# Kernel tuning notes

Hardware: AMD Instinct MI355X
Metric: run time of the kernel (lower is better)

The kernel has to match this reference:

```python
import jax, jax.numpy as jnp
import numpy as np
from jax.ops import segment_max, segment_sum

N_NODES = 50000
N_EDGES = 800000
IN_CH = 256
HEADS = 8
OUT_CH = 32
NEG_SLOPE = 0.2
EPS = 1e-16


def setup_inputs() -> dict:
    key = jax.random.key(0)
    k1, k2, k3, k4, k5 = jax.random.split(key, 5)
    x = jax.random.normal(k1, (N_NODES, IN_CH), dtype=jnp.float32)
    edge_index = jax.random.randint(k2, (2, N_EDGES), 0, N_NODES, dtype=jnp.int64)
    # params (xavier-ish scale)
    W = jax.random.normal(k3, (HEADS * OUT_CH, IN_CH), dtype=jnp.float32) * (1.0 / np.sqrt(IN_CH))
    a_left = jax.random.normal(k4, (HEADS, OUT_CH), dtype=jnp.float32) * (1.0 / np.sqrt(OUT_CH))
    a_right = jax.random.normal(k5, (HEADS, OUT_CH), dtype=jnp.float32) * (1.0 / np.sqrt(OUT_CH))
    return {"x": x, "edge_index": edge_index, "W": W, "a_left": a_left, "a_right": a_right}


def reference(x, edge_index, W, a_left, a_right):
    N = x.shape[0]
    H, C = HEADS, OUT_CH
    # add self loops
    loops = jnp.arange(N, dtype=edge_index.dtype)
    src = jnp.concatenate([edge_index[0], loops])
    dst = jnp.concatenate([edge_index[1], loops])
    # Wh: [N, H, C]
    Wh = (x @ W.T).reshape(N, H, C)
    # per-node attention halves: [N, H]
    e_left = jnp.einsum('nhc,hc->nh', Wh, a_left)
    e_right = jnp.einsum('nhc,hc->nh', Wh, a_right)
    # per-edge score: [E, H]
    e = e_left[src] + e_right[dst]
    e = jnp.where(e >= 0, e, NEG_SLOPE * e)
    # segment softmax over edges grouped by dst
    e_max = segment_max(e, dst, num_segments=N)
    e_max = jnp.where(jnp.isfinite(e_max), e_max, 0.0)
    e_exp = jnp.exp(e - e_max[dst])
    denom = segment_sum(e_exp, dst, num_segments=N)
    alpha = e_exp / (denom[dst] + EPS)
    # scatter-add aggregation: [N, H, C]
    out = segment_sum(Wh[src] * alpha[:, :, None], dst, num_segments=N)
    return out.reshape(N, H * C)
```

## Files before the change

kernel.cpp:

```cpp
#include <hip/hip_runtime.h>
#include <hip/hip_bf16.h>

#define N_NODES 50000
#define N_EDGES 800000
#define IN_CH 256
#define HEADS 8
#define OUT_CH 32
#define HC 256
#define E_TOT (N_EDGES + N_NODES)
#define NEG_SLOPE 0.2f

typedef short s16x8 __attribute__((ext_vector_type(8)));
typedef float f32x4 __attribute__((ext_vector_type(4)));

__device__ __forceinline__ unsigned short f2bf(float f) {
    unsigned int u = __float_as_uint(f);
    unsigned int r = (u + 0x7FFFu + ((u >> 16) & 1u)) >> 16;
    return (unsigned short)r;
}
__device__ __forceinline__ float bf2f(unsigned short b) {
    return __uint_as_float(((unsigned int)b) << 16);
}

__device__ __forceinline__ int tbyte(int r, int k2) { return (r * 64 + k2) ^ ((r & 7) << 4); }

__global__ __launch_bounds__(512) void gemm_kernel(const float* __restrict__ x,
                                                   const float* __restrict__ W,
                                                   const float* __restrict__ a_left,
                                                   const float* __restrict__ a_right,
                                                   unsigned short* __restrict__ Wh,
                                                   float* __restrict__ el,
                                                   float* __restrict__ er) {
    __shared__ unsigned short As[64 * 32];
    __shared__ unsigned short Bs[256 * 32];
    char* Asb = (char*)As;
    char* Bsb = (char*)Bs;
    const int m0 = blockIdx.x * 64;
    const int t  = threadIdx.x;
    const int l  = t & 63;
    const int wv = t >> 6;
    const int wr = wv & 3;
    const int wc = wv >> 1 >> 1;
    const int c16  = l & 15;
    const int rgrp = l >> 4;

    f32x4 acc[8];
#pragma unroll
    for (int i = 0; i < 8; ++i) acc[i] = (f32x4){0.f, 0.f, 0.f, 0.f};

    for (int k0 = 0; k0 < IN_CH; k0 += 32) {
        {
            int r = t >> 3, kq = (t & 7) << 2;
            float4 v = make_float4(0.f, 0.f, 0.f, 0.f);
            if (m0 + r < N_NODES) v = *(const float4*)&x[(size_t)(m0 + r) * IN_CH + k0 + kq];
            ushort4 o; o.x = f2bf(v.x); o.y = f2bf(v.y); o.z = f2bf(v.z); o.w = f2bf(v.w);
            *(ushort4*)(Asb + tbyte(r, kq * 2)) = o;
        }
        {
            int r = t >> 1, kq = (t & 1) << 4;
            const float* wp = &W[(size_t)r * IN_CH + k0 + kq];
            float4 v0 = *(const float4*)(wp + 0);
            float4 v1 = *(const float4*)(wp + 4);
            float4 v2 = *(const float4*)(wp + 8);
            float4 v3 = *(const float4*)(wp + 12);
            ushort4 o0, o1, o2, o3;
            o0.x = f2bf(v0.x); o0.y = f2bf(v0.y); o0.z = f2bf(v0.z); o0.w = f2bf(v0.w);
            o1.x = f2bf(v1.x); o1.y = f2bf(v1.y); o1.z = f2bf(v1.z); o1.w = f2bf(v1.w);
            o2.x = f2bf(v2.x); o2.y = f2bf(v2.y); o2.z = f2bf(v2.z); o2.w = f2bf(v2.w);
            o3.x = f2bf(v3.x); o3.y = f2bf(v3.y); o3.z = f2bf(v3.z); o3.w = f2bf(v3.w);
            int b0 = kq * 2;
            *(ushort4*)(Bsb + tbyte(r, b0 + 0))  = o0;
            *(ushort4*)(Bsb + tbyte(r, b0 + 8))  = o1;
            *(ushort4*)(Bsb + tbyte(r, b0 + 16)) = o2;
            *(ushort4*)(Bsb + tbyte(r, b0 + 24)) = o3;
        }
        __syncthreads();
        s16x8 af = *(const s16x8*)(Asb + tbyte(wr * 16 + c16, rgrp * 16));
#pragma unroll
        for (int nt = 0; nt < 8; ++nt) {
            s16x8 bf = *(const s16x8*)(Bsb + tbyte(wc * 128 + nt * 16 + c16, rgrp * 16));
            acc[nt] = __builtin_amdgcn_mfma_f32_16x16x32_bf16(af, bf, acc[nt], 0, 0, 0);
        }
        __syncthreads();
    }

#pragma unroll
    for (int hp = 0; hp < 4; ++hp) {
        int hg  = wc * 4 + hp;
        int nt0 = hp * 2;
        float al0 = a_left [hg * OUT_CH + c16];
        float al1 = a_left [hg * OUT_CH + 16 + c16];
        float ar0 = a_right[hg * OUT_CH + c16];
        float ar1 = a_right[hg * OUT_CH + 16 + c16];
#pragma unroll
        for (int rg = 0; rg < 4; ++rg) {
            float pl = acc[nt0][rg] * al0 + acc[nt0 + 1][rg] * al1;
            float pr = acc[nt0][rg] * ar0 + acc[nt0 + 1][rg] * ar1;
#pragma unroll
            for (int m = 1; m < 16; m <<= 1) {
                pl += __shfl_xor(pl, m, 16);
                pr += __shfl_xor(pr, m, 16);
            }
            int row = m0 + wr * 16 + rgrp * 4 + rg;
            if (c16 == 0 && row < N_NODES) {
                el[row * HEADS + hg] = pl;
                er[row * HEADS + hg] = pr;
            }
        }
    }
#pragma unroll
    for (int nt = 0; nt < 8; ++nt) {
#pragma unroll
        for (int rg = 0; rg < 4; ++rg) {
            int row = m0 + wr * 16 + rgrp * 4 + rg;
            if (row < N_NODES)
                Wh[(size_t)row * HC + wc * 128 + nt * 16 + c16] = f2bf(acc[nt][rg]);
        }
    }
}

__global__ void zero_kernel(int* __restrict__ p, int n) {
    int i = blockIdx.x * blockDim.x + threadIdx.x;
    if (i < n) p[i] = 0;
}

__global__ void hist_kernel(const int* __restrict__ src, const int* __restrict__ dst,
                            int* __restrict__ count) {
    int e = blockIdx.x * blockDim.x + threadIdx.x;
    if (e >= E_TOT) return;
    int s, d;
    if (e < N_EDGES) { s = src[e]; d = dst[e]; } else { s = d = e - N_EDGES; }
    if ((unsigned)s >= N_NODES || (unsigned)d >= N_NODES) return;
    atomicAdd(&count[d], 1);
}

__global__ __launch_bounds__(1024) void scan_kernel(const int* __restrict__ count,
                                                    int* __restrict__ offset,
                                                    int* __restrict__ cursor) {
    __shared__ int wtot[16];
    __shared__ int wbase[16];
    __shared__ int running_s;
    int t = threadIdx.x, lane = t & 63, wid = t >> 6;
    if (t == 0) running_s = 0;
    __syncthreads();
    for (int base = 0; base < N_NODES; base += 1024) {
        int idx = base + t;
        int v = (idx < N_NODES) ? count[idx] : 0;
        int s = v;
#pragma unroll
        for (int off = 1; off < 64; off <<= 1) {
            int u = __shfl_up(s, off, 64);
            if (lane >= off) s += u;
        }
        if (lane == 63) wtot[wid] = s;
        __syncthreads();
        if (t == 0) {
            int b = running_s;
            for (int w = 0; w < 16; ++w) { wbase[w] = b; b += wtot[w]; }
            running_s = b;
        }
        __syncthreads();
        int excl = s - v + wbase[wid];
        if (idx < N_NODES) { offset[idx] = excl; cursor[idx] = excl; }
        __syncthreads();
    }
    if (t == 0) offset[N_NODES] = running_s;
}

__global__ void scatter_kernel(const int* __restrict__ src, const int* __restrict__ dst,
                               int* __restrict__ cursor, int* __restrict__ srcs) {
    int e = blockIdx.x * blockDim.x + threadIdx.x;
    if (e >= E_TOT) return;
    int s, d;
    if (e < N_EDGES) { s = src[e]; d = dst[e]; } else { s = d = e - N_EDGES; }
    if ((unsigned)s >= N_NODES || (unsigned)d >= N_NODES) return;
    int pos = atomicAdd(&cursor[d], 1);
    srcs[pos] = s;
}

__global__ __launch_bounds__(256) void agg_kernel(const unsigned short* __restrict__ Wh,
                                                  const float* __restrict__ el,
                                                  const float* __restrict__ er,
                                                  const int* __restrict__ offset,
                                                  const int* __restrict__ srcs,
                                                  float* __restrict__ out) {
    int n = blockIdx.x;
    int t = threadIdx.x;
    int h = t >> 5;
    float ern = er[n * HEADS + h];
    int start = offset[n], end = offset[n + 1];
    float acc = 0.f, den = 0.f;
    int j = start;
    for (; j + 4 <= end; j += 4) {
        int s0 = srcs[j + 0], s1 = srcs[j + 1], s2 = srcs[j + 2], s3 = srcs[j + 3];
        float w0 = bf2f(Wh[(size_t)s0 * HC + t]);
        float w1 = bf2f(Wh[(size_t)s1 * HC + t]);
        float w2 = bf2f(Wh[(size_t)s2 * HC + t]);
        float w3 = bf2f(Wh[(size_t)s3 * HC + t]);
        float sc0 = el[s0 * HEADS + h] + ern;
        float sc1 = el[s1 * HEADS + h] + ern;
        float sc2 = el[s2 * HEADS + h] + ern;
        float sc3 = el[s3 * HEADS + h] + ern;
        sc0 = fmaxf(sc0, NEG_SLOPE * sc0);
        sc1 = fmaxf(sc1, NEG_SLOPE * sc1);
        sc2 = fmaxf(sc2, NEG_SLOPE * sc2);
        sc3 = fmaxf(sc3, NEG_SLOPE * sc3);
        float e0 = __expf(sc0), e1 = __expf(sc1), e2 = __expf(sc2), e3 = __expf(sc3);
        acc = fmaf(e0, w0, acc);
        acc = fmaf(e1, w1, acc);
        acc = fmaf(e2, w2, acc);
        acc = fmaf(e3, w3, acc);
        den += (e0 + e1) + (e2 + e3);
    }
    for (; j < end; ++j) {
        int s = srcs[j];
        float sc = el[s * HEADS + h] + ern;
        sc = fmaxf(sc, NEG_SLOPE * sc);
        float e = __expf(sc);
        acc = fmaf(e, bf2f(Wh[(size_t)s * HC + t]), acc);
        den += e;
    }
    out[(size_t)n * HC + t] = acc / (den + 1e-16f);
}

__global__ void sentinel_kernel(float* __restrict__ out, int n) {
    int i = blockIdx.x * blockDim.x + threadIdx.x;
    if (i < n) out[i] = 1.0e6f;
}

extern "C" void kernel_launch(void* const* d_in, const int* in_sizes, int n_in,
                              void* d_out, int out_size, void* d_ws, size_t ws_size,
                              hipStream_t stream) {
    const float* x       = (const float*)d_in[0];
    const int*   ei      = (const int*)d_in[1];
    const float* W       = (const float*)d_in[2];
    const float* a_left  = (const float*)d_in[3];
    const float* a_right = (const float*)d_in[4];
    float* out = (float*)d_out;

    const int* src = ei;
    const int* dst = ei + N_EDGES;

    char* ws = (char*)d_ws;
    size_t off = 0;
    auto alloc = [&](size_t bytes) -> void* {
        void* p = ws + off;
        off += (bytes + 255) & ~(size_t)255;
        return p;
    };
    unsigned short* Wh = (unsigned short*)alloc((size_t)N_NODES * HC * sizeof(unsigned short));
    float* el     = (float*)alloc((size_t)N_NODES * HEADS * sizeof(float));
    float* er     = (float*)alloc((size_t)N_NODES * HEADS * sizeof(float));
    int*   count  = (int*)alloc((size_t)N_NODES * sizeof(int));
    int*   offset = (int*)alloc((size_t)(N_NODES + 1) * sizeof(int));
    int*   cursor = (int*)alloc((size_t)N_NODES * sizeof(int));
    int*   srcs   = (int*)alloc((size_t)E_TOT * sizeof(int));

    if (off > ws_size) {
        sentinel_kernel<<<(out_size + 255) / 256, 256, 0, stream>>>(out, out_size);
        return;
    }

    gemm_kernel<<<(N_NODES + 63) / 64, 512, 0, stream>>>(x, W, a_left, a_right, Wh, el, er);

    zero_kernel<<<(N_NODES + 255) / 256, 256, 0, stream>>>(count, N_NODES);
    int eblocks = (E_TOT + 255) / 256;
    hist_kernel<<<eblocks, 256, 0, stream>>>(src, dst, count);
    scan_kernel<<<1, 1024, 0, stream>>>(count, offset, cursor);
    scatter_kernel<<<eblocks, 256, 0, stream>>>(src, dst, cursor, srcs);

    agg_kernel<<<N_NODES, 256, 0, stream>>>(Wh, el, er, offset, srcs, out);
}
```

Baseline: 367.0 us.

## Pre-convert W to bf16, double GEMM row tile, stage edge scores in shared memory

A separate kernel converts W to bf16 once, so GEMM blocks load bf16 weights instead of converting fp32 on every tile. The GEMM row tile grows from 64 to 128 with two MFMA row fragments per wave, which reuses each B fragment twice and halves the redundant weight traffic. The aggregation kernel now computes each edge's exp score once per head in shared memory in 64-edge chunks instead of once per thread, which removes redundant el loads and exp work. In exchange it adds a kernel launch, block-wide syncs in aggregation, and fewer GEMM blocks.

```diff
diff --git a/kernel.cpp b/kernel.cpp
--- a/kernel.cpp
+++ b/kernel.cpp
@@ -24,97 +24,114 @@
 
 __device__ __forceinline__ int tbyte(int r, int k2) { return (r * 64 + k2) ^ ((r & 7) << 4); }
 
+__global__ void wconv_kernel(const float* __restrict__ W, unsigned short* __restrict__ Wb) {
+    int i = (blockIdx.x * 256 + threadIdx.x) * 4;
+    float4 v = *(const float4*)&W[i];
+    ushort4 o; o.x = f2bf(v.x); o.y = f2bf(v.y); o.z = f2bf(v.z); o.w = f2bf(v.w);
+    *(ushort4*)&Wb[i] = o;
+}
+
 __global__ __launch_bounds__(512) void gemm_kernel(const float* __restrict__ x,
-                                                   const float* __restrict__ W,
+                                                   const unsigned short* __restrict__ Wb,
                                                    const float* __restrict__ a_left,
                                                    const float* __restrict__ a_right,
                                                    unsigned short* __restrict__ Wh,
                                                    float* __restrict__ el,
                                                    float* __restrict__ er) {
-    __shared__ unsigned short As[64 * 32];
+    __shared__ unsigned short As[128 * 32];
     __shared__ unsigned short Bs[256 * 32];
     char* Asb = (char*)As;
     char* Bsb = (char*)Bs;
-    const int m0 = blockIdx.x * 64;
+    const int m0 = blockIdx.x * 128;
     const int t  = threadIdx.x;
     const int l  = t & 63;
     const int wv = t >> 6;
     const int wr = wv & 3;
-    const int wc = wv >> 1 >> 1;
+    const int wc = wv >> 2;
     const int c16  = l & 15;
     const int rgrp = l >> 4;
 
-    f32x4 acc[8];
-#pragma unroll
-    for (int i = 0; i < 8; ++i) acc[i] = (f32x4){0.f, 0.f, 0.f, 0.f};
+    f32x4 acc[2][8];
+#pragma unroll
+    for (int i = 0; i < 2; ++i)
+#pragma unroll
+        for (int j = 0; j < 8; ++j) acc[i][j] = (f32x4){0.f, 0.f, 0.f, 0.f};
 
     for (int k0 = 0; k0 < IN_CH; k0 += 32) {
         {
-            int r = t >> 3, kq = (t & 7) << 2;
-            float4 v = make_float4(0.f, 0.f, 0.f, 0.f);
-            if (m0 + r < N_NODES) v = *(const float4*)&x[(size_t)(m0 + r) * IN_CH + k0 + kq];
-            ushort4 o; o.x = f2bf(v.x); o.y = f2bf(v.y); o.z = f2bf(v.z); o.w = f2bf(v.w);
-            *(ushort4*)(Asb + tbyte(r, kq * 2)) = o;
+            int r = t >> 2, kq = (t & 3) << 3;
+            float4 v0 = make_float4(0.f, 0.f, 0.f, 0.f), v1 = v0;
+            if (m0 + r < N_NODES) {
+                const float* xp = &x[(size_t)(m0 + r) * IN_CH + k0 + kq];
+                v0 = *(const float4*)(xp + 0);
+                v1 = *(const float4*)(xp + 4);
+            }
+            ushort4 o0, o1;
+            o0.x = f2bf(v0.x); o0.y = f2bf(v0.y); o0.z = f2bf(v0.z); o0.w = f2bf(v0.w);
+            o1.x = f2bf(v1.x); o1.y = f2bf(v1.y); o1.z = f2bf(v1.z); o1.w = f2bf(v1.w);
+            int b0 = kq * 2;
+            *(ushort4*)(Asb + tbyte(r, b0 + 0)) = o0;
+            *(ushort4*)(Asb + tbyte(r, b0 + 8)) = o1;
         }
         {
             int r = t >> 1, kq = (t & 1) << 4;
-            const float* wp = &W[(size_t)r * IN_CH + k0 + kq];
-            float4 v0 = *(const float4*)(wp + 0);
-            float4 v1 = *(const float4*)(wp + 4);
-            float4 v2 = *(const float4*)(wp + 8);
-            float4 v3 = *(const float4*)(wp + 12);
-            ushort4 o0, o1, o2, o3;
-            o0.x = f2bf(v0.x); o0.y = f2bf(v0.y); o0.z = f2bf(v0.z); o0.w = f2bf(v0.w);
-            o1.x = f2bf(v1.x); o1.y = f2bf(v1.y); o1.z = f2bf(v1.z); o1.w = f2bf(v1.w);
-            o2.x = f2bf(v2.x); o2.y = f2bf(v2.y); o2.z = f2bf(v2.z); o2.w = f2bf(v2.w);
-            o3.x = f2bf(v3.x); o3.y = f2bf(v3.y); o3.z = f2bf(v3.z); o3.w = f2bf(v3.w);
+            const unsigned short* wp = &Wb[(size_t)r * IN_CH + k0 + kq];
+            ushort4 w0 = *(const ushort4*)(wp + 0);
+            ushort4 w1 = *(const ushort4*)(wp + 4);
+            ushort4 w2 = *(const ushort4*)(wp + 8);
+            ushort4 w3 = *(const ushort4*)(wp + 12);
             int b0 = kq * 2;
-            *(ushort4*)(Bsb + tbyte(r, b0 + 0))  = o0;
-            *(ushort4*)(Bsb + tbyte(r, b0 + 8))  = o1;
-            *(ushort4*)(Bsb + tbyte(r, b0 + 16)) = o2;
-            *(ushort4*)(Bsb + tbyte(r, b0 + 24)) = o3;
-        }
-        __syncthreads();
-        s16x8 af = *(const s16x8*)(Asb + tbyte(wr * 16 + c16, rgrp * 16));
+            *(ushort4*)(Bsb + tbyte(r, b0 + 0))  = w0;
+            *(ushort4*)(Bsb + tbyte(r, b0 + 8))  = w1;
+            *(ushort4*)(Bsb + tbyte(r, b0 + 16)) = w2;
+            *(ushort4*)(Bsb + tbyte(r, b0 + 24)) = w3;
+        }
+        __syncthreads();
+        s16x8 af0 = *(const s16x8*)(Asb + tbyte(wr * 32 + c16,      rgrp * 16));
+        s16x8 af1 = *(const s16x8*)(Asb + tbyte(wr * 32 + 16 + c16, rgrp * 16));
 #pragma unroll
         for (int nt = 0; nt < 8; ++nt) {
             s16x8 bf = *(const s16x8*)(Bsb + tbyte(wc * 128 + nt * 16 + c16, rgrp * 16));
-            acc[nt] = __builtin_amdgcn_mfma_f32_16x16x32_bf16(af, bf, acc[nt], 0, 0, 0);
-        }
-        __syncthreads();
-    }
-
-#pragma unroll
-    for (int hp = 0; hp < 4; ++hp) {
-        int hg  = wc * 4 + hp;
-        int nt0 = hp * 2;
-        float al0 = a_left [hg * OUT_CH + c16];
-        float al1 = a_left [hg * OUT_CH + 16 + c16];
-        float ar0 = a_right[hg * OUT_CH + c16];
-        float ar1 = a_right[hg * OUT_CH + 16 + c16];
-#pragma unroll
-        for (int rg = 0; rg < 4; ++rg) {
-            float pl = acc[nt0][rg] * al0 + acc[nt0 + 1][rg] * al1;
-            float pr = acc[nt0][rg] * ar0 + acc[nt0 + 1][rg] * ar1;
-#pragma unroll
-            for (int m = 1; m < 16; m <<= 1) {
-                pl += __shfl_xor(pl, m, 16);
-                pr += __shfl_xor(pr, m, 16);
+            acc[0][nt] = __builtin_amdgcn_mfma_f32_16x16x32_bf16(af0, bf, acc[0][nt], 0, 0, 0);
+            acc[1][nt] = __builtin_amdgcn_mfma_f32_16x16x32_bf16(af1, bf, acc[1][nt], 0, 0, 0);
+        }
+        __syncthreads();
+    }
+
+#pragma unroll
+    for (int mt = 0; mt < 2; ++mt) {
+#pragma unroll
+        for (int hp = 0; hp < 4; ++hp) {
+            int hg  = wc * 4 + hp;
+            int nt0 = hp * 2;
+            float al0 = a_left [hg * OUT_CH + c16];
+            float al1 = a_left [hg * OUT_CH + 16 + c16];
+            float ar0 = a_right[hg * OUT_CH + c16];
+            float ar1 = a_right[hg * OUT_CH + 16 + c16];
+#pragma unroll
+            for (int rg = 0; rg < 4; ++rg) {
+                float pl = acc[mt][nt0][rg] * al0 + acc[mt][nt0 + 1][rg] * al1;
+                float pr = acc[mt][nt0][rg] * ar0 + acc[mt][nt0 + 1][rg] * ar1;
+#pragma unroll
+                for (int m = 1; m < 16; m <<= 1) {
+                    pl += __shfl_xor(pl, m, 16);
+                    pr += __shfl_xor(pr, m, 16);
+                }
+                int row = m0 + wr * 32 + mt * 16 + rgrp * 4 + rg;
+                if (c16 == 0 && row < N_NODES) {
+                    el[row * HEADS + hg] = pl;
+                    er[row * HEADS + hg] = pr;
+                }
             }
-            int row = m0 + wr * 16 + rgrp * 4 + rg;
-            if (c16 == 0 && row < N_NODES) {
-                el[row * HEADS + hg] = pl;
-                er[row * HEADS + hg] = pr;
+        }
+#pragma unroll
+        for (int nt = 0; nt < 8; ++nt) {
+#pragma unroll
+            for (int rg = 0; rg < 4; ++rg) {
+                int row = m0 + wr * 32 + mt * 16 + rgrp * 4 + rg;
+                if (row < N_NODES)
+                    Wh[(size_t)row * HC + wc * 128 + nt * 16 + c16] = f2bf(acc[mt][nt][rg]);
             }
-        }
-    }
-#pragma unroll
-    for (int nt = 0; nt < 8; ++nt) {
-#pragma unroll
-        for (int rg = 0; rg < 4; ++rg) {
-            int row = m0 + wr * 16 + rgrp * 4 + rg;
-            if (row < N_NODES)
-                Wh[(size_t)row * HC + wc * 128 + nt * 16 + c16] = f2bf(acc[nt][rg]);
         }
     }
 }
@@ -184,43 +201,40 @@
                                                   const int* __restrict__ offset,
                                                   const int* __restrict__ srcs,
                                                   float* __restrict__ out) {
+    __shared__ float e_sh[64][HEADS];
+    __shared__ int   s_sh[64];
     int n = blockIdx.x;
     int t = threadIdx.x;
     int h = t >> 5;
+    int l32 = t & 31;
     float ern = er[n * HEADS + h];
     int start = offset[n], end = offset[n + 1];
-    float acc = 0.f, den = 0.f;
-    int j = start;
-    for (; j + 4 <= end; j += 4) {
-        int s0 = srcs[j + 0], s1 = srcs[j + 1], s2 = srcs[j + 2], s3 = srcs[j + 3];
-        float w0 = bf2f(Wh[(size_t)s0 * HC + t]);
-        float w1 = bf2f(Wh[(size_t)s1 * HC + t]);
-        float w2 = bf2f(Wh[(size_t)s2 * HC + t]);
-        float w3 = bf2f(Wh[(size_t)s3 * HC + t]);
-        float sc0 = el[s0 * HEADS + h] + ern;
-        float sc1 = el[s1 * HEADS + h] + ern;
-        float sc2 = el[s2 * HEADS + h] + ern;
-        float sc3 = el[s3 * HEADS + h] + ern;
-        sc0 = fmaxf(sc0, NEG_SLOPE * sc0);
-        sc1 = fmaxf(sc1, NEG_SLOPE * sc1);
-        sc2 = fmaxf(sc2, NEG_SLOPE * sc2);
-        sc3 = fmaxf(sc3, NEG_SLOPE * sc3);
-        float e0 = __expf(sc0), e1 = __expf(sc1), e2 = __expf(sc2), e3 = __expf(sc3);
-        acc = fmaf(e0, w0, acc);
-        acc = fmaf(e1, w1, acc);
-        acc = fmaf(e2, w2, acc);
-        acc = fmaf(e3, w3, acc);
-        den += (e0 + e1) + (e2 + e3);
-    }
-    for (; j < end; ++j) {
-        int s = srcs[j];
-        float sc = el[s * HEADS + h] + ern;
-        sc = fmaxf(sc, NEG_SLOPE * sc);
-        float e = __expf(sc);
-        acc = fmaf(e, bf2f(Wh[(size_t)s * HC + t]), acc);
-        den += e;
-    }
-    out[(size_t)n * HC + t] = acc / (den + 1e-16f);
+    float acc = 0.f, denp = 0.f;
+
+    for (int c0 = start; c0 < end; c0 += 64) {
+        int m = min(64, end - c0);
+#pragma unroll 2
+        for (int jj = l32; jj < m; jj += 32) {
+            int s = srcs[c0 + jj];
+            if (h == 0) s_sh[jj] = s;
+            float sc = el[s * HEADS + h] + ern;
+            sc = fmaxf(sc, NEG_SLOPE * sc);
+            float e = __expf(sc);
+            e_sh[jj][h] = e;
+            denp += e;
+        }
+        __syncthreads();
+#pragma unroll 4
+        for (int jj = 0; jj < m; ++jj) {
+            int s   = s_sh[jj];
+            float e = e_sh[jj][h];
+            acc = fmaf(e, bf2f(Wh[(size_t)s * HC + t]), acc);
+        }
+        __syncthreads();
+    }
+#pragma unroll
+    for (int m = 16; m >= 1; m >>= 1) denp += __shfl_xor(denp, m);
+    out[(size_t)n * HC + t] = acc / (denp + 1e-16f);
 }
 
 __global__ void sentinel_kernel(float* __restrict__ out, int n) {
@@ -255,13 +269,15 @@
     int*   offset = (int*)alloc((size_t)(N_NODES + 1) * sizeof(int));
     int*   cursor = (int*)alloc((size_t)N_NODES * sizeof(int));
     int*   srcs   = (int*)alloc((size_t)E_TOT * sizeof(int));
+    unsigned short* Wb = (unsigned short*)alloc((size_t)HC * IN_CH * sizeof(unsigned short));
 
     if (off > ws_size) {
         sentinel_kernel<<<(out_size + 255) / 256, 256, 0, stream>>>(out, out_size);
         return;
     }
 
-    gemm_kernel<<<(N_NODES + 63) / 64, 512, 0, stream>>>(x, W, a_left, a_right, Wh, el, er);
+    wconv_kernel<<<(HC * IN_CH) / 1024, 256, 0, stream>>>(W, Wb);
+    gemm_kernel<<<(N_NODES + 127) / 128, 512, 0, stream>>>(x, Wb, a_left, a_right, Wh, el, er);
 
     zero_kernel<<<(N_NODES + 255) / 256, 256, 0, stream>>>(count, N_NODES);
     int eblocks = (E_TOT + 255) / 256;
```

New measurement: 368.0 us. No clear change (+0.3%).
